# Optimization experiments

Measured on AMD Instinct MI355X. Metric: run time of the kernel, lower is better.

## Reference

```python
import jax, jax.numpy as jnp
import numpy as np

N = 20000        # nodes
E = 640000       # edges (before self-loops)
F_IN = 128
HID = 64
HEADS = 4
F_OUT = 128
G = 64           # graphs in batch
NEG_SLOPE = 0.2  # PyG GATConv leaky_relu default


def setup_inputs() -> dict:
    key = jax.random.key(0)
    ks = jax.random.split(key, 16)
    s = 0.05
    x = jax.random.normal(ks[0], (N, F_IN), jnp.float32)
    edge_index = jax.random.randint(ks[1], (2, E), 0, N, dtype=jnp.int64)
    batch = jnp.sort(jax.random.randint(ks[2], (N,), 0, G, dtype=jnp.int64))
    # layer 1: F_IN -> HID x HEADS (concat)
    W1 = jax.random.normal(ks[3], (F_IN, HEADS * HID), jnp.float32) * s
    a_src1 = jax.random.normal(ks[4], (HEADS, HID), jnp.float32) * s
    a_dst1 = jax.random.normal(ks[5], (HEADS, HID), jnp.float32) * s
    b1 = jnp.zeros((HEADS * HID,), jnp.float32)
    # layer 2: HEADS*HID -> HID x HEADS (concat)
    W2 = jax.random.normal(ks[6], (HEADS * HID, HEADS * HID), jnp.float32) * s
    a_src2 = jax.random.normal(ks[7], (HEADS, HID), jnp.float32) * s
    a_dst2 = jax.random.normal(ks[8], (HEADS, HID), jnp.float32) * s
    b2 = jnp.zeros((HEADS * HID,), jnp.float32)
    # layer 3: HEADS*HID -> F_OUT, heads=1, concat=False (mean)
    W3 = jax.random.normal(ks[9], (HEADS * HID, F_OUT), jnp.float32) * s
    a_src3 = jax.random.normal(ks[10], (1, F_OUT), jnp.float32) * s
    a_dst3 = jax.random.normal(ks[11], (1, F_OUT), jnp.float32) * s
    b3 = jnp.zeros((F_OUT,), jnp.float32)
    return dict(x=x, edge_index=edge_index, batch=batch,
                W1=W1, a_src1=a_src1, a_dst1=a_dst1, b1=b1,
                W2=W2, a_src2=a_src2, a_dst2=a_dst2, b2=b2,
                W3=W3, a_src3=a_src3, a_dst3=a_dst3, b3=b3)


def _gat_layer(x, src, dst, W, a_s, a_d, b, heads, concat):
    n = x.shape[0]
    h = (x @ W).reshape(n, heads, -1)                # [N,H,C]
    alpha_s = (h * a_s[None]).sum(-1)                # [N,H]
    alpha_d = (h * a_d[None]).sum(-1)                # [N,H]
    e = jax.nn.leaky_relu(alpha_s[src] + alpha_d[dst], NEG_SLOPE)  # [E,H]
    # segment softmax over incoming edges of each dst node
    m = jax.ops.segment_max(e, dst, num_segments=n)
    ex = jnp.exp(e - m[dst])
    denom = jax.ops.segment_sum(ex, dst, num_segments=n)
    alpha = ex / (denom[dst] + 1e-16)                # [E,H]
    out = jax.ops.segment_sum(alpha[:, :, None] * h[src], dst, num_segments=n)  # [N,H,C]
    out = out.reshape(n, -1) if concat else out.mean(axis=1)
    return out + b


def reference(x, edge_index, batch, W1, a_src1, a_dst1, b1,
              W2, a_src2, a_dst2, b2, W3, a_src3, a_dst3, b3):
    n = x.shape[0]
    # add self loops (PyG GATConv default add_self_loops=True)
    loop = jnp.arange(n, dtype=edge_index.dtype)
    src = jnp.concatenate([edge_index[0], loop])
    dst = jnp.concatenate([edge_index[1], loop])

    h = _gat_layer(x, src, dst, W1, a_src1, a_dst1, b1, HEADS, True)
    h = jax.nn.elu(h)
    h = _gat_layer(h, src, dst, W2, a_src2, a_dst2, b2, HEADS, True)
    h = jax.nn.elu(h)
    h = _gat_layer(h, src, dst, W3, a_src3, a_dst3, b3, 1, False)

    # global mean pool over graphs
    sums = jax.ops.segment_sum(h, batch, num_segments=G)
    cnts = jax.ops.segment_sum(jnp.ones((n, 1), h.dtype), batch, num_segments=G)
    graph_embedding = sums / jnp.maximum(cnts, 1.0)
    return graph_embedding, h
```

## Files before the change

kernel.cpp:

```cpp
#include <hip/hip_runtime.h>
#include <hip/hip_bf16.h>
#include <math.h>

#define N_NODES 20000
#define N_EDGES 640000
#define ET_EDGES (N_EDGES + N_NODES)
#define G_GRAPHS 64
#define NEG_SLOPE 0.2f

typedef __attribute__((ext_vector_type(8))) short s8v;
typedef __attribute__((ext_vector_type(4))) float f4v;

__device__ __forceinline__ unsigned short bf_hi(float f) {
    union { float f; unsigned int u; } c; c.f = f;
    unsigned int r = (c.u + 0x7fffu + ((c.u >> 16) & 1u)) >> 16;
    return (unsigned short)r;
}
__device__ __forceinline__ float bf_f(unsigned short h) {
    union { unsigned int u; float f; } c; c.u = ((unsigned int)h) << 16;
    return c.f;
}


__global__ void hist_dst(const int* __restrict__ ei, int* __restrict__ cnt,
                         const int* __restrict__ batch, int* __restrict__ gstart) {
    int j = blockIdx.x * blockDim.x + threadIdx.x;
    if (blockIdx.x == 0 && threadIdx.x <= G_GRAPHS) {
        int g = threadIdx.x;
        int lo = 0, hi = N_NODES;
        while (lo < hi) {
            int mid = (lo + hi) >> 1;
            if (batch[mid] < g) lo = mid + 1; else hi = mid;
        }
        gstart[g] = lo;
    }
    if (j >= ET_EDGES) return;
    int d = (j < N_EDGES) ? ei[N_EDGES + j] : (j - N_EDGES);
    atomicAdd(&cnt[d], 1);
}

__global__ __launch_bounds__(1024) void scan_rowptr(const int* __restrict__ cnt,
                                                    int* __restrict__ row_ptr) {
    __shared__ int sums[1024];
    const int n = N_NODES;
    const int CH = (n + 1023) / 1024;
    int t = threadIdx.x;
    int base = t * CH;
    int s = 0;
    for (int i = 0; i < CH; ++i) {
        int idx = base + i;
        if (idx < n) s += cnt[idx];
    }
    sums[t] = s;
    __syncthreads();
    for (int o = 1; o < 1024; o <<= 1) {
        int v = (t >= o) ? sums[t - o] : 0;
        __syncthreads();
        sums[t] += v;
        __syncthreads();
    }
    int run = (t == 0) ? 0 : sums[t - 1];
    for (int i = 0; i < CH; ++i) {
        int idx = base + i;
        if (idx < n) { row_ptr[idx] = run; run += cnt[idx]; }
    }
    if (t == 1023) row_ptr[n] = sums[1023];
}

__global__ void fill_csr(const int* __restrict__ ei, const int* __restrict__ row_ptr,
                         int* __restrict__ cur, int* __restrict__ col) {
    int j = blockIdx.x * blockDim.x + threadIdx.x;
    if (j >= ET_EDGES) return;
    int s, d;
    if (j < N_EDGES) { s = ei[j]; d = ei[N_EDGES + j]; }
    else             { s = d = j - N_EDGES; }
    int pos = row_ptr[d] + atomicAdd(&cur[d], 1);
    col[pos] = s;
}


__global__ void prep_split(const float* __restrict__ x,
                           const float* __restrict__ W1, const float* __restrict__ W2,
                           const float* __restrict__ W3,
                           unsigned short* __restrict__ xh, unsigned short* __restrict__ xl,
                           unsigned short* __restrict__ w1h, unsigned short* __restrict__ w1l,
                           unsigned short* __restrict__ w2h, unsigned short* __restrict__ w2l,
                           unsigned short* __restrict__ w3h, unsigned short* __restrict__ w3l,
                           int* __restrict__ cntcur, float* __restrict__ gout,
                           float* __restrict__ alphaz) {
    int idx = blockIdx.x * blockDim.x + threadIdx.x;
    if (idx < 640000) {
        int i = idx * 4;
        float4 v = *(const float4*)&x[i];
        ushort4 h, l;
        h.x = bf_hi(v.x); l.x = bf_hi(v.x - bf_f(h.x));
        h.y = bf_hi(v.y); l.y = bf_hi(v.y - bf_f(h.y));
        h.z = bf_hi(v.z); l.z = bf_hi(v.z - bf_f(h.z));
        h.w = bf_hi(v.w); l.w = bf_hi(v.w - bf_f(h.w));
        *(ushort4*)&xh[i] = h;
        *(ushort4*)&xl[i] = l;
        return;
    }
    idx -= 640000;
    if (idx < 32768) {
        int k = idx / 256, n = idx % 256;
        float v = W1[idx];
        unsigned short h = bf_hi(v);
        w1h[n * 128 + k] = h;
        w1l[n * 128 + k] = bf_hi(v - bf_f(h));
        return;
    }
    idx -= 32768;
    if (idx < 65536) {
        int k = idx / 256, n = idx % 256;
        float v = W2[idx];
        unsigned short h = bf_hi(v);
        w2h[n * 256 + k] = h;
        w2l[n * 256 + k] = bf_hi(v - bf_f(h));
        return;
    }
    idx -= 65536;
    if (idx < 32768) {
        int k = idx / 128, n = idx % 128;
        float v = W3[idx];
        unsigned short h = bf_hi(v);
        w3h[n * 256 + k] = h;
        w3l[n * 256 + k] = bf_hi(v - bf_f(h));
        return;
    }
    idx -= 32768;
    if (idx < 10000) {
        *(int4*)&cntcur[idx * 4] = make_int4(0, 0, 0, 0);
        return;
    }
    idx -= 10000;
    if (idx < 2048) {
        *(float4*)&gout[idx * 4] = make_float4(0.f, 0.f, 0.f, 0.f);
        return;
    }
    idx -= 2048;
    if (idx < 90000) {
        *(float4*)&alphaz[idx * 4] = make_float4(0.f, 0.f, 0.f, 0.f);
    }
}


#define LDT 40

template <int CPH>
__global__ __launch_bounds__(256) void gemm_split(
        const unsigned short* __restrict__ Ah, const unsigned short* __restrict__ Al,
        const unsigned short* __restrict__ Bh, const unsigned short* __restrict__ Bl,
        float* __restrict__ C, int M, int Nc, int K,
        const float* __restrict__ a_src, const float* __restrict__ a_dst,
        float* __restrict__ asT, float* __restrict__ adT) {
    __shared__ unsigned short lAh[128 * LDT];
    __shared__ unsigned short lAl[128 * LDT];
    __shared__ unsigned short lBh[64 * LDT];
    __shared__ unsigned short lBl[64 * LDT];
    int bm = blockIdx.x * 128, bn = blockIdx.y * 64;
    int t = threadIdx.x, w = t >> 6, lane = t & 63;
    int wm = (w >> 1) * 64, wn = (w & 1) * 32;

    f4v acc[4][2] = {};

    int sr = t >> 1, sk = (t & 1) << 4;
    int br = t >> 2, bk = (t & 3) << 3;
    int ar = bm + sr; if (ar >= M) ar = M - 1;
    const unsigned short* pAh = Ah + (size_t)ar * K + sk;
    const unsigned short* pAl = Al + (size_t)ar * K + sk;
    const unsigned short* pBh = Bh + (size_t)(bn + br) * K + bk;
    const unsigned short* pBl = Bl + (size_t)(bn + br) * K + bk;

    int fr = lane & 15, fk = (lane >> 4) << 3;

    for (int k0 = 0; k0 < K; k0 += 32) {
        uint4 vh0 = *(const uint4*)(pAh + k0);
        uint4 vh1 = *(const uint4*)(pAh + k0 + 8);
        uint4 vl0 = *(const uint4*)(pAl + k0);
        uint4 vl1 = *(const uint4*)(pAl + k0 + 8);
        uint4 wh  = *(const uint4*)(pBh + k0);
        uint4 wl  = *(const uint4*)(pBl + k0);
        __syncthreads();
        *(uint4*)&lAh[sr * LDT + sk]     = vh0;
        *(uint4*)&lAh[sr * LDT + sk + 8] = vh1;
        *(uint4*)&lAl[sr * LDT + sk]     = vl0;
        *(uint4*)&lAl[sr * LDT + sk + 8] = vl1;
        *(uint4*)&lBh[br * LDT + bk] = wh;
        *(uint4*)&lBl[br * LDT + bk] = wl;
        __syncthreads();

        s8v a_h[4], a_l[4], b_h[2], b_l[2];
        #pragma unroll
        for (int mi = 0; mi < 4; ++mi) {
            a_h[mi] = *(const s8v*)&lAh[(wm + mi * 16 + fr) * LDT + fk];
            a_l[mi] = *(const s8v*)&lAl[(wm + mi * 16 + fr) * LDT + fk];
        }
        #pragma unroll
        for (int nj = 0; nj < 2; ++nj) {
            b_h[nj] = *(const s8v*)&lBh[(wn + nj * 16 + fr) * LDT + fk];
            b_l[nj] = *(const s8v*)&lBl[(wn + nj * 16 + fr) * LDT + fk];
        }
        #pragma unroll
        for (int mi = 0; mi < 4; ++mi)
            #pragma unroll
            for (int nj = 0; nj < 2; ++nj) {
                acc[mi][nj] = __builtin_amdgcn_mfma_f32_16x16x32_bf16(
                    a_h[mi], b_h[nj], acc[mi][nj], 0, 0, 0);
                acc[mi][nj] = __builtin_amdgcn_mfma_f32_16x16x32_bf16(
                    a_h[mi], b_l[nj], acc[mi][nj], 0, 0, 0);
                acc[mi][nj] = __builtin_amdgcn_mfma_f32_16x16x32_bf16(
                    a_l[mi], b_h[nj], acc[mi][nj], 0, 0, 0);
            }
    }

    #pragma unroll
    for (int mi = 0; mi < 4; ++mi)
        #pragma unroll
        for (int nj = 0; nj < 2; ++nj) {
            int row0 = bm + wm + mi * 16 + (lane >> 4) * 4;
            int colc = bn + wn + nj * 16 + (lane & 15);
            #pragma unroll
            for (int q = 0; q < 4; ++q) {
                int r = row0 + q;
                if (r < M) C[(size_t)r * Nc + colc] = acc[mi][nj][q];
            }
        }

    float av_s[2], av_d[2];
    #pragma unroll
    for (int nj = 0; nj < 2; ++nj) {
        int aidx = bn + wn + nj * 16 + fr;
        av_s[nj] = a_src[aidx];
        av_d[nj] = a_dst[aidx];
    }
    int head = bn / CPH;
    #pragma unroll
    for (int mi = 0; mi < 4; ++mi) {
        #pragma unroll
        for (int q = 0; q < 4; ++q) {
            float ps = acc[mi][0][q] * av_s[0] + acc[mi][1][q] * av_s[1];
            float pd = acc[mi][0][q] * av_d[0] + acc[mi][1][q] * av_d[1];
            #pragma unroll
            for (int o = 1; o < 16; o <<= 1) {
                ps += __shfl_xor(ps, o);
                pd += __shfl_xor(pd, o);
            }
            if (fr == 0) {
                int r = bm + wm + mi * 16 + (lane >> 4) * 4 + q;
                if (r < M) {
                    atomicAdd(&asT[(size_t)head * M + r], ps);
                    atomicAdd(&adT[(size_t)head * M + r], pd);
                }
            }
        }
    }
}


template <int NSLICE, int SCH, int F, int HEADS, bool DO_ELU, bool SPLIT>
__global__ __launch_bounds__(256) void gat_aggregate_sliced(
        const float* __restrict__ h,
        const float* __restrict__ asT,
        const float* __restrict__ adT,
        const int* __restrict__ row_ptr,
        const int* __restrict__ col,
        const float* __restrict__ bias,
        float* __restrict__ out,
        unsigned short* __restrict__ oh,
        unsigned short* __restrict__ ol) {
    constexpr int CL = SCH / 4;
    constexpr int E  = 64 / CL;
    constexpr int CPH = F / HEADS;
    __shared__ int   s_off[4][64];
    __shared__ float s_p[4][64];
    int slice = blockIdx.x & (NSLICE - 1);
    int ng = blockIdx.x >> 2;
    int wid = threadIdx.x >> 6, lane = threadIdx.x & 63;
    int v = ng * 4 + wid;
    if (v >= N_NODES) return;
    int head = (slice * SCH) / CPH;
    int eg = lane / CL, cl = lane % CL;
    int r0 = row_ptr[v], r1 = row_ptr[v + 1];
    float ad = adT[head * N_NODES + v];
    const float* asrc = asT + head * N_NODES;
    float acc[4] = {};
    float lsum = 0.f;
    const char* hb = (const char*)(h + slice * SCH + cl * 4);

#define GATHER4(gg)                                                        \
    {                                                                      \
        int k0 = ((gg) + 0) * E + eg;                                      \
        int k1 = ((gg) + 1) * E + eg;                                      \
        int k2 = ((gg) + 2) * E + eg;                                      \
        int k3 = ((gg) + 3) * E + eg;                                      \
        float p0 = s_p[wid][k0]; int o0 = s_off[wid][k0];                  \
        float p1 = s_p[wid][k1]; int o1 = s_off[wid][k1];                  \
        float p2 = s_p[wid][k2]; int o2 = s_off[wid][k2];                  \
        float p3 = s_p[wid][k3]; int o3 = s_off[wid][k3];                  \
        float4 h0 = *(const float4*)(hb + o0);                             \
        float4 h1 = *(const float4*)(hb + o1);                             \
        float4 h2 = *(const float4*)(hb + o2);                             \
        float4 h3 = *(const float4*)(hb + o3);                             \
        acc[0] = fmaf(p0, h0.x, acc[0]);                                   \
        acc[1] = fmaf(p0, h0.y, acc[1]);                                   \
        acc[2] = fmaf(p0, h0.z, acc[2]);                                   \
        acc[3] = fmaf(p0, h0.w, acc[3]);                                   \
        acc[0] = fmaf(p1, h1.x, acc[0]);                                   \
        acc[1] = fmaf(p1, h1.y, acc[1]);                                   \
        acc[2] = fmaf(p1, h1.z, acc[2]);                                   \
        acc[3] = fmaf(p1, h1.w, acc[3]);                                   \
        acc[0] = fmaf(p2, h2.x, acc[0]);                                   \
        acc[1] = fmaf(p2, h2.y, acc[1]);                                   \
        acc[2] = fmaf(p2, h2.z, acc[2]);                                   \
        acc[3] = fmaf(p2, h2.w, acc[3]);                                   \
        acc[0] = fmaf(p3, h3.x, acc[0]);                                   \
        acc[1] = fmaf(p3, h3.y, acc[1]);                                   \
        acc[2] = fmaf(p3, h3.z, acc[2]);                                   \
        acc[3] = fmaf(p3, h3.w, acc[3]);                                   \
    }

    for (int base = r0; base < r1; base += 64) {
        int j = base + lane;
        bool valid = j < r1;
        int s = col[valid ? j : r0];
        float e = asrc[s] + ad;
        e = (e > 0.f) ? e : NEG_SLOPE * e;
        float p = valid ? __expf(e) : 0.f;
        lsum += p;
        s_p[wid][lane] = p;
        s_off[wid][lane] = s * (F * 4);

        int nk = min(64, r1 - base);
        int nkg = (nk + E - 1) / E;
        int g = 0;
        for (; g + 4 <= nkg; g += 4) GATHER4(g);
        if (g < nkg) GATHER4(g);
    }
#undef GATHER4

    #pragma unroll
    for (int o = 32; o; o >>= 1) lsum += __shfl_xor(lsum, o);
    #pragma unroll
    for (int c = 0; c < 4; ++c) {
        #pragma unroll
        for (int o = CL; o < 64; o <<= 1) acc[c] += __shfl_xor(acc[c], o);
    }
    if (eg == 0) {
        float inv = 1.f / (lsum + 1e-16f);
        int ch0 = slice * SCH + cl * 4;
        float o4[4];
        #pragma unroll
        for (int c = 0; c < 4; ++c) {
            float o = acc[c] * inv + bias[ch0 + c];
            if (DO_ELU) o = (o > 0.f) ? o : expm1f(o);
            o4[c] = o;
        }
        if constexpr (SPLIT) {
            ushort4 hv4, lv4;
            hv4.x = bf_hi(o4[0]); lv4.x = bf_hi(o4[0] - bf_f(hv4.x));
            hv4.y = bf_hi(o4[1]); lv4.y = bf_hi(o4[1] - bf_f(hv4.y));
            hv4.z = bf_hi(o4[2]); lv4.z = bf_hi(o4[2] - bf_f(hv4.z));
            hv4.w = bf_hi(o4[3]); lv4.w = bf_hi(o4[3] - bf_f(hv4.w));
            *(ushort4*)&oh[(size_t)v * F + ch0] = hv4;
            *(ushort4*)&ol[(size_t)v * F + ch0] = lv4;
        } else {
            *(float4*)&out[(size_t)v * F + ch0] =
                make_float4(o4[0], o4[1], o4[2], o4[3]);
        }
    }
}


__global__ void pool_mean4(const float* __restrict__ hout, const int* __restrict__ gstart,
                           float* __restrict__ gout) {
    int g = blockIdx.x;
    int q = blockIdx.y;
    int c = threadIdx.x;
    int off = gstart[g], end = gstart[g + 1];
    float inv = 1.f / fmaxf((float)(end - off), 1.0f);
    float s = 0.f;
    for (int i = off + q; i < end; i += 4) s += hout[(size_t)i * 128 + c];
    atomicAdd(&gout[g * 128 + c], s * inv);
}


static inline size_t align_up(size_t x, size_t a) { return (x + a - 1) & ~(a - 1); }

extern "C" void kernel_launch(void* const* d_in, const int* in_sizes, int n_in,
                              void* d_out, int out_size, void* d_ws, size_t ws_size,
                              hipStream_t stream) {
    const float* x   = (const float*)d_in[0];
    const int*   ei  = (const int*)d_in[1];
    const int*   bat = (const int*)d_in[2];
    const float* W1  = (const float*)d_in[3];
    const float* as1 = (const float*)d_in[4];
    const float* ad1 = (const float*)d_in[5];
    const float* b1  = (const float*)d_in[6];
    const float* W2  = (const float*)d_in[7];
    const float* as2 = (const float*)d_in[8];
    const float* ad2 = (const float*)d_in[9];
    const float* b2  = (const float*)d_in[10];
    const float* W3  = (const float*)d_in[11];
    const float* as3 = (const float*)d_in[12];
    const float* ad3 = (const float*)d_in[13];
    const float* b3  = (const float*)d_in[14];

    float* gout = (float*)d_out;
    float* hout = (float*)d_out + G_GRAPHS * 128;

    char* w = (char*)d_ws;
    size_t o = 0;
    float* bufA = (float*)(w + o);           o = align_up(o + (size_t)N_NODES * 256 * 4, 256);
    unsigned short* Bh = (unsigned short*)(w + o); o = align_up(o + (size_t)N_NODES * 256 * 2, 256);
    unsigned short* Bl = (unsigned short*)(w + o); o = align_up(o + (size_t)N_NODES * 256 * 2, 256);
    unsigned short* xh = (unsigned short*)(w + o); o = align_up(o + (size_t)N_NODES * 128 * 2, 256);
    unsigned short* xl = (unsigned short*)(w + o); o = align_up(o + (size_t)N_NODES * 128 * 2, 256);
    unsigned short* Wt1h = (unsigned short*)(w + o); o = align_up(o + (size_t)256 * 128 * 2, 256);
    unsigned short* Wt1l = (unsigned short*)(w + o); o = align_up(o + (size_t)256 * 128 * 2, 256);
    unsigned short* Wt2h = (unsigned short*)(w + o); o = align_up(o + (size_t)256 * 256 * 2, 256);
    unsigned short* Wt2l = (unsigned short*)(w + o); o = align_up(o + (size_t)256 * 256 * 2, 256);
    unsigned short* Wt3h = (unsigned short*)(w + o); o = align_up(o + (size_t)128 * 256 * 2, 256);
    unsigned short* Wt3l = (unsigned short*)(w + o); o = align_up(o + (size_t)128 * 256 * 2, 256);
    float* alpha = (float*)(w + o);
    float* asv1 = alpha;
    float* adv1 = alpha + 4 * N_NODES;
    float* asv2 = alpha + 8 * N_NODES;
    float* adv2 = alpha + 12 * N_NODES;
    float* asv3 = alpha + 16 * N_NODES;
    float* adv3 = alpha + 17 * N_NODES;
    o = align_up(o + (size_t)18 * N_NODES * 4, 256);
    int* row_ptr = (int*)(w + o);  o = align_up(o + (size_t)(N_NODES + 1) * 4, 256);
    int* col     = (int*)(w + o);  o = align_up(o + (size_t)ET_EDGES * 4, 256);
    int* cnt     = (int*)(w + o);  o += (size_t)N_NODES * 4;
    int* cur     = (int*)(w + o);  o = align_up(o + (size_t)N_NODES * 4, 256);
    int* gstart  = (int*)(w + o);  o = align_up(o + (size_t)(G_GRAPHS + 1) * 4, 256);

    {
        int total = 640000 + 32768 + 65536 + 32768 + 10000 + 2048 + 90000;
        prep_split<<<(total + 255) / 256, 256, 0, stream>>>(
            x, W1, W2, W3, xh, xl, Wt1h, Wt1l, Wt2h, Wt2l, Wt3h, Wt3l, cnt, gout, alpha);
    }
    hist_dst<<<(ET_EDGES + 255) / 256, 256, 0, stream>>>(ei, cnt, bat, gstart);
    scan_rowptr<<<1, 1024, 0, stream>>>(cnt, row_ptr);
    fill_csr<<<(ET_EDGES + 255) / 256, 256, 0, stream>>>(ei, row_ptr, cur, col);

    int gm = (N_NODES + 127) / 128;
    int nb = (N_NODES + 3) / 4;
    int nbs = nb * 4;

    gemm_split<64><<<dim3(gm, 4), 256, 0, stream>>>(
        xh, xl, Wt1h, Wt1l, bufA, N_NODES, 256, 128, as1, ad1, asv1, adv1);
    gat_aggregate_sliced<4, 64, 256, 4, true, true><<<nbs, 256, 0, stream>>>(
        bufA, asv1, adv1, row_ptr, col, b1, nullptr, Bh, Bl);

    gemm_split<64><<<dim3(gm, 4), 256, 0, stream>>>(
        Bh, Bl, Wt2h, Wt2l, bufA, N_NODES, 256, 256, as2, ad2, asv2, adv2);
    gat_aggregate_sliced<4, 64, 256, 4, true, true><<<nbs, 256, 0, stream>>>(
        bufA, asv2, adv2, row_ptr, col, b2, nullptr, Bh, Bl);

    gemm_split<128><<<dim3(gm, 2), 256, 0, stream>>>(
        Bh, Bl, Wt3h, Wt3l, bufA, N_NODES, 128, 256, as3, ad3, asv3, adv3);
    gat_aggregate_sliced<4, 32, 128, 1, false, false><<<nbs, 256, 0, stream>>>(
        bufA, asv3, adv3, row_ptr, col, b3, hout, nullptr, nullptr);

    pool_mean4<<<dim3(G_GRAPHS, 4), 128, 0, stream>>>(hout, gstart, gout);
}
```

Measured before the change: 426.0 us.

## Store projected features in fp16 and fuse mean pooling into final aggregation

The GEMM output buffer holding projected node features is now stored as fp16 instead of fp32, which halves the bytes gathered per edge in the aggregation kernels; each lane now handles 8 channels via 16-byte loads. The separate pool_mean kernel is removed and the final aggregation atomically adds its per-node contributions, scaled by the graph's inverse node count, into the graph embedding. The fp16 storage loses precision in the features used for aggregation. The fused pooling does per-node atomics, which may contend on the 64 graph rows.

```diff
diff --git a/kernel.cpp b/kernel.cpp
--- a/kernel.cpp
+++ b/kernel.cpp
@@ -1,5 +1,6 @@
 #include <hip/hip_runtime.h>
 #include <hip/hip_bf16.h>
+#include <hip/hip_fp16.h>
 #include <math.h>
 
 #define N_NODES 20000
@@ -151,7 +152,7 @@
 __global__ __launch_bounds__(256) void gemm_split(
         const unsigned short* __restrict__ Ah, const unsigned short* __restrict__ Al,
         const unsigned short* __restrict__ Bh, const unsigned short* __restrict__ Bl,
-        float* __restrict__ C, int M, int Nc, int K,
+        __half* __restrict__ C, int M, int Nc, int K,
         const float* __restrict__ a_src, const float* __restrict__ a_dst,
         float* __restrict__ asT, float* __restrict__ adT) {
     __shared__ unsigned short lAh[128 * LDT];
@@ -223,7 +224,7 @@
             #pragma unroll
             for (int q = 0; q < 4; ++q) {
                 int r = row0 + q;
-                if (r < M) C[(size_t)r * Nc + colc] = acc[mi][nj][q];
+                if (r < M) C[(size_t)r * Nc + colc] = __float2half(acc[mi][nj][q]);
             }
         }
 
@@ -258,9 +259,9 @@
 }
 
 
-template <int NSLICE, int SCH, int F, int HEADS, bool DO_ELU, bool SPLIT>
-__global__ __launch_bounds__(256) void gat_aggregate_sliced(
-        const float* __restrict__ h,
+template <int SCH, int F, int HEADS, bool DO_ELU, bool SPLIT, bool POOL>
+__global__ __launch_bounds__(256) void gat_aggregate6(
+        const __half* __restrict__ h,
         const float* __restrict__ asT,
         const float* __restrict__ adT,
         const int* __restrict__ row_ptr,
@@ -268,13 +269,16 @@
         const float* __restrict__ bias,
         float* __restrict__ out,
         unsigned short* __restrict__ oh,
-        unsigned short* __restrict__ ol) {
-    constexpr int CL = SCH / 4;
+        unsigned short* __restrict__ ol,
+        const int* __restrict__ batch,
+        const int* __restrict__ gstart,
+        float* __restrict__ gout) {
+    constexpr int CL = SCH / 8;
     constexpr int E  = 64 / CL;
     constexpr int CPH = F / HEADS;
     __shared__ int   s_off[4][64];
     __shared__ float s_p[4][64];
-    int slice = blockIdx.x & (NSLICE - 1);
+    int slice = blockIdx.x & 3;
     int ng = blockIdx.x >> 2;
     int wid = threadIdx.x >> 6, lane = threadIdx.x & 63;
     int v = ng * 4 + wid;
@@ -284,9 +288,20 @@
     int r0 = row_ptr[v], r1 = row_ptr[v + 1];
     float ad = adT[head * N_NODES + v];
     const float* asrc = asT + head * N_NODES;
-    float acc[4] = {};
+    float acc[8] = {};
     float lsum = 0.f;
-    const char* hb = (const char*)(h + slice * SCH + cl * 4);
+    const char* hb = (const char*)h + (slice * SCH + cl * 8) * 2;
+
+#define HFMA(pk, hw)                                                       \
+    { const __half2* q2 = (const __half2*)&(hw);                           \
+      float2 f0 = __half22float2(q2[0]);                                   \
+      float2 f1 = __half22float2(q2[1]);                                   \
+      float2 f2 = __half22float2(q2[2]);                                   \
+      float2 f3 = __half22float2(q2[3]);                                   \
+      acc[0] = fmaf(pk, f0.x, acc[0]); acc[1] = fmaf(pk, f0.y, acc[1]);    \
+      acc[2] = fmaf(pk, f1.x, acc[2]); acc[3] = fmaf(pk, f1.y, acc[3]);    \
+      acc[4] = fmaf(pk, f2.x, acc[4]); acc[5] = fmaf(pk, f2.y, acc[5]);    \
+      acc[6] = fmaf(pk, f3.x, acc[6]); acc[7] = fmaf(pk, f3.y, acc[7]); }
 
 #define GATHER4(gg)                                                        \
     {                                                                      \
@@ -298,26 +313,11 @@
         float p1 = s_p[wid][k1]; int o1 = s_off[wid][k1];                  \
         float p2 = s_p[wid][k2]; int o2 = s_off[wid][k2];                  \
         float p3 = s_p[wid][k3]; int o3 = s_off[wid][k3];                  \
-        float4 h0 = *(const float4*)(hb + o0);                             \
-        float4 h1 = *(const float4*)(hb + o1);                             \
-        float4 h2 = *(const float4*)(hb + o2);                             \
-        float4 h3 = *(const float4*)(hb + o3);                             \
-        acc[0] = fmaf(p0, h0.x, acc[0]);                                   \
-        acc[1] = fmaf(p0, h0.y, acc[1]);                                   \
-        acc[2] = fmaf(p0, h0.z, acc[2]);                                   \
-        acc[3] = fmaf(p0, h0.w, acc[3]);                                   \
-        acc[0] = fmaf(p1, h1.x, acc[0]);                                   \
-        acc[1] = fmaf(p1, h1.y, acc[1]);                                   \
-        acc[2] = fmaf(p1, h1.z, acc[2]);                                   \
-        acc[3] = fmaf(p1, h1.w, acc[3]);                                   \
-        acc[0] = fmaf(p2, h2.x, acc[0]);                                   \
-        acc[1] = fmaf(p2, h2.y, acc[1]);                                   \
-        acc[2] = fmaf(p2, h2.z, acc[2]);                                   \
-        acc[3] = fmaf(p2, h2.w, acc[3]);                                   \
-        acc[0] = fmaf(p3, h3.x, acc[0]);                                   \
-        acc[1] = fmaf(p3, h3.y, acc[1]);                                   \
-        acc[2] = fmaf(p3, h3.z, acc[2]);                                   \
-        acc[3] = fmaf(p3, h3.w, acc[3]);                                   \
+        uint4 h0 = *(const uint4*)(hb + o0);                               \
+        uint4 h1 = *(const uint4*)(hb + o1);                               \
+        uint4 h2 = *(const uint4*)(hb + o2);                               \
+        uint4 h3 = *(const uint4*)(hb + o3);                               \
+        HFMA(p0, h0); HFMA(p1, h1); HFMA(p2, h2); HFMA(p3, h3);            \
     }
 
     for (int base = r0; base < r1; base += 64) {
@@ -329,7 +329,7 @@
         float p = valid ? __expf(e) : 0.f;
         lsum += p;
         s_p[wid][lane] = p;
-        s_off[wid][lane] = s * (F * 4);
+        s_off[wid][lane] = s * (F * 2);
 
         int nk = min(64, r1 - base);
         int nkg = (nk + E - 1) / E;
@@ -338,50 +338,46 @@
         if (g < nkg) GATHER4(g);
     }
 #undef GATHER4
+#undef HFMA
 
     #pragma unroll
     for (int o = 32; o; o >>= 1) lsum += __shfl_xor(lsum, o);
     #pragma unroll
-    for (int c = 0; c < 4; ++c) {
+    for (int c = 0; c < 8; ++c) {
         #pragma unroll
         for (int o = CL; o < 64; o <<= 1) acc[c] += __shfl_xor(acc[c], o);
     }
     if (eg == 0) {
         float inv = 1.f / (lsum + 1e-16f);
-        int ch0 = slice * SCH + cl * 4;
-        float o4[4];
-        #pragma unroll
-        for (int c = 0; c < 4; ++c) {
+        int ch0 = slice * SCH + cl * 8;
+        float o8[8];
+        #pragma unroll
+        for (int c = 0; c < 8; ++c) {
             float o = acc[c] * inv + bias[ch0 + c];
             if (DO_ELU) o = (o > 0.f) ? o : expm1f(o);
-            o4[c] = o;
+            o8[c] = o;
         }
         if constexpr (SPLIT) {
-            ushort4 hv4, lv4;
-            hv4.x = bf_hi(o4[0]); lv4.x = bf_hi(o4[0] - bf_f(hv4.x));
-            hv4.y = bf_hi(o4[1]); lv4.y = bf_hi(o4[1] - bf_f(hv4.y));
-            hv4.z = bf_hi(o4[2]); lv4.z = bf_hi(o4[2] - bf_f(hv4.z));
-            hv4.w = bf_hi(o4[3]); lv4.w = bf_hi(o4[3] - bf_f(hv4.w));
-            *(ushort4*)&oh[(size_t)v * F + ch0] = hv4;
-            *(ushort4*)&ol[(size_t)v * F + ch0] = lv4;
+            unsigned short hv[8], lv[8];
+            #pragma unroll
+            for (int c = 0; c < 8; ++c) {
+                hv[c] = bf_hi(o8[c]);
+                lv[c] = bf_hi(o8[c] - bf_f(hv[c]));
+            }
+            *(uint4*)&oh[(size_t)v * F + ch0] = *(const uint4*)hv;
+            *(uint4*)&ol[(size_t)v * F + ch0] = *(const uint4*)lv;
         } else {
-            *(float4*)&out[(size_t)v * F + ch0] =
-                make_float4(o4[0], o4[1], o4[2], o4[3]);
-        }
-    }
-}
-
-
-__global__ void pool_mean4(const float* __restrict__ hout, const int* __restrict__ gstart,
-                           float* __restrict__ gout) {
-    int g = blockIdx.x;
-    int q = blockIdx.y;
-    int c = threadIdx.x;
-    int off = gstart[g], end = gstart[g + 1];
-    float inv = 1.f / fmaxf((float)(end - off), 1.0f);
-    float s = 0.f;
-    for (int i = off + q; i < end; i += 4) s += hout[(size_t)i * 128 + c];
-    atomicAdd(&gout[g * 128 + c], s * inv);
+            *(float4*)&out[(size_t)v * F + ch0]     = *(const float4*)&o8[0];
+            *(float4*)&out[(size_t)v * F + ch0 + 4] = *(const float4*)&o8[4];
+        }
+        if constexpr (POOL) {
+            int g = batch[v];
+            float invc = 1.f / fmaxf((float)(gstart[g + 1] - gstart[g]), 1.0f);
+            #pragma unroll
+            for (int c = 0; c < 8; ++c)
+                atomicAdd(&gout[g * 128 + ch0 + c], o8[c] * invc);
+        }
+    }
 }
 
 
@@ -411,7 +407,7 @@
 
     char* w = (char*)d_ws;
     size_t o = 0;
-    float* bufA = (float*)(w + o);           o = align_up(o + (size_t)N_NODES * 256 * 4, 256);
+    __half* bufA = (__half*)(w + o);         o = align_up(o + (size_t)N_NODES * 256 * 2, 256);
     unsigned short* Bh = (unsigned short*)(w + o); o = align_up(o + (size_t)N_NODES * 256 * 2, 256);
     unsigned short* Bl = (unsigned short*)(w + o); o = align_up(o + (size_t)N_NODES * 256 * 2, 256);
     unsigned short* xh = (unsigned short*)(w + o); o = align_up(o + (size_t)N_NODES * 128 * 2, 256);
@@ -451,18 +447,16 @@
 
     gemm_split<64><<<dim3(gm, 4), 256, 0, stream>>>(
         xh, xl, Wt1h, Wt1l, bufA, N_NODES, 256, 128, as1, ad1, asv1, adv1);
-    gat_aggregate_sliced<4, 64, 256, 4, true, true><<<nbs, 256, 0, stream>>>(
-        bufA, asv1, adv1, row_ptr, col, b1, nullptr, Bh, Bl);
+    gat_aggregate6<64, 256, 4, true, true, false><<<nbs, 256, 0, stream>>>(
+        bufA, asv1, adv1, row_ptr, col, b1, nullptr, Bh, Bl, nullptr, nullptr, nullptr);
 
     gemm_split<64><<<dim3(gm, 4), 256, 0, stream>>>(
         Bh, Bl, Wt2h, Wt2l, bufA, N_NODES, 256, 256, as2, ad2, asv2, adv2);
-    gat_aggregate_sliced<4, 64, 256, 4, true, true><<<nbs, 256, 0, stream>>>(
-        bufA, asv2, adv2, row_ptr, col, b2, nullptr, Bh, Bl);
+    gat_aggregate6<64, 256, 4, true, true, false><<<nbs, 256, 0, stream>>>(
+        bufA, asv2, adv2, row_ptr, col, b2, nullptr, Bh, Bl, nullptr, nullptr, nullptr);
 
     gemm_split<128><<<dim3(gm, 2), 256, 0, stream>>>(
         Bh, Bl, Wt3h, Wt3l, bufA, N_NODES, 128, 256, as3, ad3, asv3, adv3);
-    gat_aggregate_sliced<4, 32, 128, 1, false, false><<<nbs, 256, 0, stream>>>(
-        bufA, asv3, adv3, row_ptr, col, b3, hout, nullptr, nullptr);
-
-    pool_mean4<<<dim3(G_GRAPHS, 4), 128, 0, stream>>>(hout, gstart, gout);
-}
+    gat_aggregate6<32, 128, 1, false, false, true><<<nbs, 256, 0, stream>>>(
+        bufA, asv3, adv3, row_ptr, col, b3, hout, nullptr, nullptr, bat, gstart, gout);
+}
```

Result: slower. 708.9 us (+66.4%).
